# Optimization experiments

Hardware: AMD Instinct MI355X
Metric: run time of the kernel (lower is better)

Reference implementation:

```python
import jax, jax.numpy as jnp
import numpy as np

LOG_DT_MIN = float(np.log(0.001))
LOG_DT_MAX = float(np.log(0.1))


def setup_inputs() -> dict:
    key = jax.random.key(0)
    k1, k2, k3, k4 = jax.random.split(key, 4)
    H, n = 1024, 32  # n = state_dim // 2
    log_dt = jax.random.uniform(k1, (H,), dtype=jnp.float32) * (LOG_DT_MAX - LOG_DT_MIN) + LOG_DT_MIN
    C_re = jax.random.normal(k2, (H, n), dtype=jnp.float32)
    C_im = jax.random.normal(k3, (H, n), dtype=jnp.float32)
    log_A_re = jax.random.normal(k4, (H, n), dtype=jnp.float32)
    A_im = jnp.ones((H, n), dtype=jnp.float32)
    return {"log_dt": log_dt, "C_re": C_re, "C_im": C_im,
            "log_A_re": log_A_re, "A_im": A_im, "L": 4096}


def reference(log_dt, C_re, C_im, log_A_re, A_im, L):
    dt = jnp.exp(log_dt)                       # (H,)
    C = C_re + 1j * C_im                       # (H, n) complex64
    A = -jnp.exp(log_A_re) + 1j * A_im         # (H, n) complex64
    dtA = A * dt[:, None]                      # (H, n)
    # Vandermonde: exp(dtA) ** l for l in [0, L)
    K = dtA[:, :, None] * jnp.arange(L, dtype=jnp.float32)  # (H, n, L)
    C = C * (jnp.exp(dtA) - 1.0) / A           # (H, n)
    return 2.0 * jnp.einsum('hn,hnl->hl', C, jnp.exp(K)).real  # (H, L)
```

## Files before the change

kernel.cpp:

```cpp
#include <hip/hip_runtime.h>
#include <math.h>

#define BLOCK 128
#define CHUNK 32

typedef float f32x2 __attribute__((ext_vector_type(2)));

__global__ __launch_bounds__(BLOCK) void s4_vandermonde(
    const float* __restrict__ log_dt,
    const float* __restrict__ C_re,
    const float* __restrict__ C_im,
    const float* __restrict__ log_A_re,
    const float* __restrict__ A_im,
    float* __restrict__ out,
    int n, int L)
{
    const int h    = blockIdx.x;
    const int base = blockIdx.y * (BLOCK * CHUNK);
    const int tid  = threadIdx.x;

    extern __shared__ float smem[];
    float* s_x  = smem;
    float* s_y  = s_x  + n;
    float* s_cr = s_y  + n;
    float* s_ci = s_cr + n;
    float* s_wr = s_ci + n;
    float* s_wi = s_wr + n;
    float* s_a  = s_wi + n;
    float* s_nb = s_a  + n;

    for (int i = tid; i < n; i += BLOCK) {
        const float dt  = __expf(log_dt[h]);
        const float Are = -__expf(log_A_re[(size_t)h * n + i]);
        const float Aim = A_im[(size_t)h * n + i];
        const float x = Are * dt;
        const float y = Aim * dt;

        float ex = __expf(x), sy, cy;
        __sincosf(y, &sy, &cy);
        const float er = ex * cy, ei = ex * sy;

        const float numr = er - 1.0f, numi = ei;
        const float inv  = 1.0f / (Are * Are + Aim * Aim);
        const float dr = (numr * Are + numi * Aim) * inv;
        const float di = (numi * Are - numr * Aim) * inv;
        const float Cr = C_re[(size_t)h * n + i];
        const float Ci = C_im[(size_t)h * n + i];
        s_cr[i] = Cr * dr - Ci * di;
        s_ci[i] = Cr * di + Ci * dr;
        s_x[i] = x;
        s_y[i] = y;

        float exs = __expf(x * (float)BLOCK), ss, cs;
        __sincosf(y * (float)BLOCK, &ss, &cs);
        const float Wr = exs * cs, Wi = exs * ss;
        s_wr[i] = Wr;
        s_wi[i] = Wi;
        s_a[i]  = 2.0f * Wr;
        s_nb[i] = -(exs * exs);
    }
    __syncthreads();

    f32x2 acc[CHUNK];
#pragma unroll
    for (int j = 0; j < CHUNK; ++j) acc[j] = (f32x2)(0.0f);

    const float fl = (float)(base + tid);
    const int npair = n >> 1;

    for (int p = 0; p < npair; ++p) {
        const int i0 = 2 * p, i1 = 2 * p + 1;
        f32x2 rp, rc;
        {
            const float x = s_x[i0], y = s_y[i0];
            float e0 = __expf(x * fl), s0, c0;
            __sincosf(y * fl, &s0, &c0);
            const float cr = s_cr[i0], ci = s_ci[i0];
            const float sr = e0 * (cr * c0 - ci * s0);
            const float si = e0 * (cr * s0 + ci * c0);
            rp.x = sr;
            rc.x = sr * s_wr[i0] - si * s_wi[i0];
        }
        {
            const float x = s_x[i1], y = s_y[i1];
            float e0 = __expf(x * fl), s0, c0;
            __sincosf(y * fl, &s0, &c0);
            const float cr = s_cr[i1], ci = s_ci[i1];
            const float sr = e0 * (cr * c0 - ci * s0);
            const float si = e0 * (cr * s0 + ci * c0);
            rp.y = sr;
            rc.y = sr * s_wr[i1] - si * s_wi[i1];
        }
        const f32x2 a01  = { s_a[i0],  s_a[i1] };
        const f32x2 nb01 = { s_nb[i0], s_nb[i1] };

        acc[0] += rp;
        acc[1] += rc;
#pragma unroll
        for (int j = 2; j < CHUNK; ++j) {
            const f32x2 rn = __builtin_elementwise_fma(a01, rc, nb01 * rp);
            acc[j] += rn;
            rp = rc;
            rc = rn;
        }
    }
    if (n & 1) {
        const int i = n - 1;
        const float x = s_x[i], y = s_y[i];
        float e0 = __expf(x * fl), s0, c0;
        __sincosf(y * fl, &s0, &c0);
        const float cr = s_cr[i], ci = s_ci[i];
        const float sr = e0 * (cr * c0 - ci * s0);
        const float si = e0 * (cr * s0 + ci * c0);
        float rp = sr;
        float rc = sr * s_wr[i] - si * s_wi[i];
        const float a = s_a[i], nb = s_nb[i];
        acc[0].x += rp;
        acc[1].x += rc;
#pragma unroll
        for (int j = 2; j < CHUNK; ++j) {
            const float rn = fmaf(a, rc, nb * rp);
            acc[j].x += rn;
            rp = rc;
            rc = rn;
        }
    }

    float* o = out + (size_t)h * L + base + tid;
#pragma unroll
    for (int j = 0; j < CHUNK; ++j) {
        const int l = base + tid + j * BLOCK;
        if (l < L) o[(size_t)j * BLOCK] = 2.0f * (acc[j].x + acc[j].y);
    }
}

extern "C" void kernel_launch(void* const* d_in, const int* in_sizes, int n_in,
                              void* d_out, int out_size, void* d_ws, size_t ws_size,
                              hipStream_t stream) {
    const float* log_dt   = (const float*)d_in[0];
    const float* C_re     = (const float*)d_in[1];
    const float* C_im     = (const float*)d_in[2];
    const float* log_A_re = (const float*)d_in[3];
    const float* A_im     = (const float*)d_in[4];
    float* out = (float*)d_out;

    const int H = in_sizes[0];
    const int n = in_sizes[1] / H;
    const int L = out_size / H;

    const int lchunks = (L + BLOCK * CHUNK - 1) / (BLOCK * CHUNK);
    dim3 grid(H, lchunks);
    const size_t lds = (size_t)8 * n * sizeof(float);
    s4_vandermonde<<<grid, BLOCK, lds, stream>>>(
        log_dt, C_re, C_im, log_A_re, A_im, out, n, L);
}
```

Before: 80.04 us.

## Split state modes across two thread groups and reduce partial sums through LDS

Result: no change. 80.14 us (+0.1%).

```diff
diff --git a/kernel.cpp b/kernel.cpp
--- a/kernel.cpp
+++ b/kernel.cpp
@@ -1,12 +1,14 @@
 #include <hip/hip_runtime.h>
 #include <math.h>
 
-#define BLOCK 128
+#define BLOCK 256
+#define LANES 128
 #define CHUNK 32
+#define NGROUP 2
 
 typedef float f32x2 __attribute__((ext_vector_type(2)));
 
-__global__ __launch_bounds__(BLOCK) void s4_vandermonde(
+__global__ __launch_bounds__(BLOCK, 4) void s4_vandermonde(
     const float* __restrict__ log_dt,
     const float* __restrict__ C_re,
     const float* __restrict__ C_im,
@@ -16,18 +18,22 @@
     int n, int L)
 {
     const int h    = blockIdx.x;
-    const int base = blockIdx.y * (BLOCK * CHUNK);
+    const int base = blockIdx.y * (LANES * CHUNK);
     const int tid  = threadIdx.x;
+    const int grp  = tid >> 7;
+    const int lane = tid & (LANES - 1);
 
     extern __shared__ float smem[];
+    const int ns = (n + 1) & ~1;
     float* s_x  = smem;
-    float* s_y  = s_x  + n;
-    float* s_cr = s_y  + n;
-    float* s_ci = s_cr + n;
-    float* s_wr = s_ci + n;
-    float* s_wi = s_wr + n;
-    float* s_a  = s_wi + n;
-    float* s_nb = s_a  + n;
+    float* s_y  = s_x  + ns;
+    float* s_cr = s_y  + ns;
+    float* s_ci = s_cr + ns;
+    float* s_wr = s_ci + ns;
+    float* s_wi = s_wr + ns;
+    float* s_a  = s_wi + ns;
+    float* s_nb = s_a  + ns;
+    float* s_part = s_nb + ns;
 
     for (int i = tid; i < n; i += BLOCK) {
         const float dt  = __expf(log_dt[h]);
@@ -51,60 +57,83 @@
         s_x[i] = x;
         s_y[i] = y;
 
-        float exs = __expf(x * (float)BLOCK), ss, cs;
-        __sincosf(y * (float)BLOCK, &ss, &cs);
-        const float Wr = exs * cs, Wi = exs * ss;
-        s_wr[i] = Wr;
-        s_wi[i] = Wi;
-        s_a[i]  = 2.0f * Wr;
+        float exs = __expf(x * (float)LANES), ss, cs;
+        __sincosf(y * (float)LANES, &ss, &cs);
+        s_wr[i] = exs * cs;
+        s_wi[i] = exs * ss;
+        s_a[i]  = 2.0f * exs * cs;
         s_nb[i] = -(exs * exs);
     }
     __syncthreads();
 
-    f32x2 acc[CHUNK];
+    const f32x2* x2  = (const f32x2*)s_x;
+    const f32x2* y2  = (const f32x2*)s_y;
+    const f32x2* cr2 = (const f32x2*)s_cr;
+    const f32x2* ci2 = (const f32x2*)s_ci;
+    const f32x2* wr2 = (const f32x2*)s_wr;
+    const f32x2* wi2 = (const f32x2*)s_wi;
+    const f32x2* a2  = (const f32x2*)s_a;
+    const f32x2* nb2 = (const f32x2*)s_nb;
+
+    float acc[CHUNK];
 #pragma unroll
-    for (int j = 0; j < CHUNK; ++j) acc[j] = (f32x2)(0.0f);
+    for (int j = 0; j < CHUNK; ++j) acc[j] = 0.0f;
 
-    const float fl = (float)(base + tid);
+    const float fl = (float)(base + lane);
     const int npair = n >> 1;
+    const int p0 = (npair * grp) / NGROUP;
+    const int p1 = (npair * (grp + 1)) / NGROUP;
 
-    for (int p = 0; p < npair; ++p) {
-        const int i0 = 2 * p, i1 = 2 * p + 1;
-        f32x2 rp, rc;
-        {
-            const float x = s_x[i0], y = s_y[i0];
-            float e0 = __expf(x * fl), s0, c0;
-            __sincosf(y * fl, &s0, &c0);
-            const float cr = s_cr[i0], ci = s_ci[i0];
-            const float sr = e0 * (cr * c0 - ci * s0);
-            const float si = e0 * (cr * s0 + ci * c0);
-            rp.x = sr;
-            rc.x = sr * s_wr[i0] - si * s_wi[i0];
-        }
-        {
-            const float x = s_x[i1], y = s_y[i1];
-            float e0 = __expf(x * fl), s0, c0;
-            __sincosf(y * fl, &s0, &c0);
-            const float cr = s_cr[i1], ci = s_ci[i1];
-            const float sr = e0 * (cr * c0 - ci * s0);
-            const float si = e0 * (cr * s0 + ci * c0);
-            rp.y = sr;
-            rc.y = sr * s_wr[i1] - si * s_wi[i1];
-        }
-        const f32x2 a01  = { s_a[i0],  s_a[i1] };
-        const f32x2 nb01 = { s_nb[i0], s_nb[i1] };
+#define INIT_PAIR(p, rp, rc, a, nb)                                    \
+    {                                                                  \
+        const f32x2 xf = x2[p] * fl;                                   \
+        const f32x2 yf = y2[p] * fl;                                   \
+        float e0 = __expf(xf.x), e1 = __expf(xf.y);                    \
+        float sn0, cs0, sn1, cs1;                                      \
+        __sincosf(yf.x, &sn0, &cs0);                                   \
+        __sincosf(yf.y, &sn1, &cs1);                                   \
+        const f32x2 e  = { e0, e1 };                                   \
+        const f32x2 sn = { sn0, sn1 };                                 \
+        const f32x2 cs = { cs0, cs1 };                                 \
+        const f32x2 cr = cr2[p], ci = ci2[p];                          \
+        const f32x2 sr = e * (cr * cs - ci * sn);                      \
+        const f32x2 si = e * (cr * sn + ci * cs);                      \
+        rp = sr;                                                       \
+        rc = sr * wr2[p] - si * wi2[p];                                \
+        a  = a2[p];                                                    \
+        nb = nb2[p];                                                   \
+    }
 
-        acc[0] += rp;
-        acc[1] += rc;
+    int p = p0;
+    for (; p + 1 < p1; p += 2) {
+        f32x2 rpA, rcA, aA, nbA, rpB, rcB, aB, nbB;
+        INIT_PAIR(p,     rpA, rcA, aA, nbA);
+        INIT_PAIR(p + 1, rpB, rcB, aB, nbB);
+        acc[0] += (rpA.x + rpA.y) + (rpB.x + rpB.y);
+        acc[1] += (rcA.x + rcA.y) + (rcB.x + rcB.y);
 #pragma unroll
         for (int j = 2; j < CHUNK; ++j) {
-            const f32x2 rn = __builtin_elementwise_fma(a01, rc, nb01 * rp);
-            acc[j] += rn;
-            rp = rc;
-            rc = rn;
+            const f32x2 rnA = __builtin_elementwise_fma(aA, rcA, nbA * rpA);
+            const f32x2 rnB = __builtin_elementwise_fma(aB, rcB, nbB * rpB);
+            const f32x2 t = rnA + rnB;
+            acc[j] += t.x + t.y;
+            rpA = rcA; rcA = rnA;
+            rpB = rcB; rcB = rnB;
         }
     }
-    if (n & 1) {
+    if (p < p1) {
+        f32x2 rp_, rc_, a_, nb_;
+        INIT_PAIR(p, rp_, rc_, a_, nb_);
+        acc[0] += rp_.x + rp_.y;
+        acc[1] += rc_.x + rc_.y;
+#pragma unroll
+        for (int j = 2; j < CHUNK; ++j) {
+            const f32x2 rn = __builtin_elementwise_fma(a_, rc_, nb_ * rp_);
+            acc[j] += rn.x + rn.y;
+            rp_ = rc_; rc_ = rn;
+        }
+    }
+    if ((n & 1) && grp == NGROUP - 1) {
         const int i = n - 1;
         const float x = s_x[i], y = s_y[i];
         float e0 = __expf(x * fl), s0, c0;
@@ -112,25 +141,34 @@
         const float cr = s_cr[i], ci = s_ci[i];
         const float sr = e0 * (cr * c0 - ci * s0);
         const float si = e0 * (cr * s0 + ci * c0);
-        float rp = sr;
-        float rc = sr * s_wr[i] - si * s_wi[i];
-        const float a = s_a[i], nb = s_nb[i];
-        acc[0].x += rp;
-        acc[1].x += rc;
+        float rp_ = sr;
+        float rc_ = sr * s_wr[i] - si * s_wi[i];
+        const float a_ = s_a[i], nb_ = s_nb[i];
+        acc[0] += rp_;
+        acc[1] += rc_;
 #pragma unroll
         for (int j = 2; j < CHUNK; ++j) {
-            const float rn = fmaf(a, rc, nb * rp);
-            acc[j].x += rn;
-            rp = rc;
-            rc = rn;
+            const float rn = fmaf(a_, rc_, nb_ * rp_);
+            acc[j] += rn;
+            rp_ = rc_;
+            rc_ = rn;
         }
     }
+#undef INIT_PAIR
 
-    float* o = out + (size_t)h * L + base + tid;
+    if (grp == 1) {
 #pragma unroll
-    for (int j = 0; j < CHUNK; ++j) {
-        const int l = base + tid + j * BLOCK;
-        if (l < L) o[(size_t)j * BLOCK] = 2.0f * (acc[j].x + acc[j].y);
+        for (int j = 0; j < CHUNK; ++j)
+            s_part[j * LANES + lane] = acc[j];
+    }
+    __syncthreads();
+    if (grp == 0) {
+        float* o = out + (size_t)h * L + base + lane;
+#pragma unroll
+        for (int j = 0; j < CHUNK; ++j) {
+            const int l = base + lane + j * LANES;
+            if (l < L) o[(size_t)j * LANES] = 2.0f * (acc[j] + s_part[j * LANES + lane]);
+        }
     }
 }
 
@@ -148,9 +186,10 @@
     const int n = in_sizes[1] / H;
     const int L = out_size / H;
 
-    const int lchunks = (L + BLOCK * CHUNK - 1) / (BLOCK * CHUNK);
+    const int lchunks = (L + LANES * CHUNK - 1) / (LANES * CHUNK);
     dim3 grid(H, lchunks);
-    const size_t lds = (size_t)8 * n * sizeof(float);
+    const int ns = (n + 1) & ~1;
+    const size_t lds = ((size_t)8 * ns + (size_t)CHUNK * LANES) * sizeof(float);
     s4_vandermonde<<<grid, BLOCK, lds, stream>>>(
         log_dt, C_re, C_im, log_A_re, A_im, out, n, L);
 }
```
